# Performance work log

Measured on AMD Instinct MI355X. Metric: run time of the kernel, lower is better.

The kernel has to match this reference:

```python
import jax, jax.numpy as jnp
import numpy as np

D_MODEL = 1024
N_HEADS = 16
HEAD_DIM = D_MODEL // N_HEADS


def setup_inputs() -> dict:
    key = jax.random.key(0)
    ks = jax.random.split(key, 10)
    s = 1.0 / np.sqrt(D_MODEL)
    inp = {
        "ts_features": jax.random.normal(ks[0], (8, 512, D_MODEL), dtype=jnp.float32),
        "llm_features": jax.random.normal(ks[1], (8, 2048, D_MODEL), dtype=jnp.float32),
        "q_w": jax.random.uniform(ks[2], (D_MODEL, D_MODEL), jnp.float32, -s, s),
        "q_b": jax.random.uniform(ks[3], (D_MODEL,), jnp.float32, -s, s),
        "k_w": jax.random.uniform(ks[4], (D_MODEL, D_MODEL), jnp.float32, -s, s),
        "k_b": jax.random.uniform(ks[5], (D_MODEL,), jnp.float32, -s, s),
        "v_w": jax.random.uniform(ks[6], (D_MODEL, D_MODEL), jnp.float32, -s, s),
        "v_b": jax.random.uniform(ks[7], (D_MODEL,), jnp.float32, -s, s),
        "o_w": jax.random.uniform(ks[8], (D_MODEL, D_MODEL), jnp.float32, -s, s),
        "o_b": jax.random.uniform(ks[9], (D_MODEL,), jnp.float32, -s, s),
    }
    return inp


def reference(ts_features, llm_features, q_w, q_b, k_w, k_b, v_w, v_b, o_w, o_b):
    B, P, _ = ts_features.shape
    S = llm_features.shape[1]
    # Linear projections (torch Linear: x @ W^T + b); split heads -> [B, H, L, Dh]
    q = (ts_features @ q_w.T + q_b).reshape(B, P, N_HEADS, HEAD_DIM).transpose(0, 2, 1, 3)
    k = (llm_features @ k_w.T + k_b).reshape(B, S, N_HEADS, HEAD_DIM).transpose(0, 2, 1, 3)
    v = (llm_features @ v_w.T + v_b).reshape(B, S, N_HEADS, HEAD_DIM).transpose(0, 2, 1, 3)
    # Full attention: scores [B, H, P, S]
    scores = jnp.einsum("bhpd,bhsd->bhps", q, k) / np.sqrt(HEAD_DIM).astype(np.float32)
    attn = jax.nn.softmax(scores, axis=-1)  # dropout is identity in eval mode
    context = jnp.einsum("bhps,bhsd->bhpd", attn, v)
    context = context.transpose(0, 2, 1, 3).reshape(B, P, D_MODEL)
    return context @ o_w.T + o_b
```

## Files before the change

### kernel.cpp

```cpp
#include <hip/hip_runtime.h>

#define DM 1024
#define B_ 8
#define P_ 512
#define S_ 2048

typedef __bf16 bf16;
typedef __bf16 bf16x4 __attribute__((ext_vector_type(4)));
typedef __bf16 bf16x8 __attribute__((ext_vector_type(8)));
typedef float f32x4 __attribute__((ext_vector_type(4)));
typedef float f32x16 __attribute__((ext_vector_type(16)));

__device__ __forceinline__ void gload_lds16(const void* g, void* l) {
  __builtin_amdgcn_global_load_lds(
      (const __attribute__((address_space(1))) unsigned int*)g,
      (__attribute__((address_space(3))) unsigned int*)l, 16, 0, 0);
}

__device__ __forceinline__ f32x4 mfma16(bf16x8 a, bf16x8 b, f32x4 c) {
  return __builtin_amdgcn_mfma_f32_16x16x32_bf16(a, b, c, 0, 0, 0);
}
__device__ __forceinline__ f32x16 mfma32(bf16x8 a, bf16x8 b, f32x16 c) {
  return __builtin_amdgcn_mfma_f32_32x32x16_bf16(a, b, c, 0, 0, 0);
}

__device__ __forceinline__ unsigned cvt_pk_bf16(float lo, float hi) {
  unsigned r;
  asm("v_cvt_pk_bf16_f32 %0, %1, %2" : "=v"(r) : "v"(lo), "v"(hi));
  return r;
}
__device__ __forceinline__ void plswap(unsigned& a, unsigned& b) {
  asm volatile("s_nop 1\n\tv_permlane32_swap_b32 %0, %1" : "+v"(a), "+v"(b));
}
__device__ __forceinline__ void bar() {
  asm volatile("" ::: "memory");
  __builtin_amdgcn_s_barrier();
  asm volatile("" ::: "memory");
}

union U8 { unsigned u[4]; bf16x8 v; };

#define QSCALE 0.18033688011112042f

__global__ void cvt_all(const float* __restrict__ ts, const float* __restrict__ llm,
                        const float* __restrict__ qw, const float* __restrict__ kw,
                        const float* __restrict__ vw, const float* __restrict__ ow,
                        bf16* __restrict__ ts_o, bf16* __restrict__ llm_o,
                        bf16* __restrict__ qw_o, bf16* __restrict__ kw_o,
                        bf16* __restrict__ vw_o, bf16* __restrict__ ow_o) {
  const int total = 24 << 18;
  int i = blockIdx.x * blockDim.x + threadIdx.x;
  const int stride = gridDim.x * blockDim.x;
  for (; i < total; i += stride) {
    int r = i >> 18;
    const float* in;
    bf16* out;
    int off;
    if (r < 4) { in = ts; out = ts_o; off = i; }
    else if (r < 20) { in = llm; out = llm_o; off = i - (4 << 18); }
    else if (r == 20) { in = qw; out = qw_o; off = i - (20 << 18); }
    else if (r == 21) { in = kw; out = kw_o; off = i - (21 << 18); }
    else if (r == 22) { in = vw; out = vw_o; off = i - (22 << 18); }
    else { in = ow; out = ow_o; off = i - (23 << 18); }
    float4 v = reinterpret_cast<const float4*>(in)[off];
    bf16x4 o;
    o[0] = (bf16)v.x; o[1] = (bf16)v.y; o[2] = (bf16)v.z; o[3] = (bf16)v.w;
    reinterpret_cast<bf16x4*>(out)[off] = o;
  }
}

enum { MODE_F32 = 0, MODE_Q = 1 };

template <int MODE>
__global__ __launch_bounds__(512) void gemm_bt(
    const bf16* __restrict__ A, const bf16* __restrict__ Bw,
    const float* __restrict__ bias, void* __restrict__ out) {
  __shared__ char As[16384];
  __shared__ char Bs[16384];
  const int tid = threadIdx.x;
  const int w = tid >> 6, lane = tid & 63;
  const int g = lane >> 4, l15 = lane & 15;
  const int tn = blockIdx.x, tm = blockIdx.y;
  const int wm = w >> 2, wn = w & 3;

  f32x4 acc[4][2] = {};

  const char* Abase = (const char*)A + (size_t)(tm * 128) * (DM * 2);
  const char* Bbase = (const char*)Bw + (size_t)(tn * 128) * (DM * 2);

  for (int kt = 0; kt < DM / 64; ++kt) {
#pragma unroll
    for (int i = 0; i < 2; ++i) {
      int f = i * 8192 + (w * 64 + lane) * 16;
      int row = f >> 7;
      int kb = f & 127;
      int src = kb ^ ((row & 7) << 4);
      gload_lds16(Abase + (size_t)row * (DM * 2) + kt * 128 + src,
                  As + i * 8192 + w * 1024);
      gload_lds16(Bbase + (size_t)row * (DM * 2) + kt * 128 + src,
                  Bs + i * 8192 + w * 1024);
    }
    __syncthreads();
#pragma unroll
    for (int kk = 0; kk < 2; ++kk) {
      bf16x8 af[4], bfr[2];
#pragma unroll
      for (int mi = 0; mi < 4; ++mi) {
        int row = wm * 64 + mi * 16 + l15;
        int off = row * 128 + ((kk * 64 + g * 16) ^ ((row & 7) << 4));
        af[mi] = *reinterpret_cast<const bf16x8*>(As + off);
      }
#pragma unroll
      for (int ni = 0; ni < 2; ++ni) {
        int row = wn * 32 + ni * 16 + l15;
        int off = row * 128 + ((kk * 64 + g * 16) ^ ((row & 7) << 4));
        bfr[ni] = *reinterpret_cast<const bf16x8*>(Bs + off);
      }
#pragma unroll
      for (int mi = 0; mi < 4; ++mi)
#pragma unroll
        for (int ni = 0; ni < 2; ++ni)
          acc[mi][ni] = mfma16(af[mi], bfr[ni], acc[mi][ni]);
    }
    __syncthreads();
  }

#pragma unroll
  for (int mi = 0; mi < 4; ++mi) {
#pragma unroll
    for (int ni = 0; ni < 2; ++ni) {
      const int n = tn * 128 + wn * 32 + ni * 16 + l15;
      const float bn = bias[n];
      const int mb = tm * 128 + wm * 64 + mi * 16 + g * 4;
#pragma unroll
      for (int r = 0; r < 4; ++r) {
        const int m = mb + r;
        const float v = acc[mi][ni][r] + bn;
        if constexpr (MODE == MODE_F32) {
          ((float*)out)[(size_t)m * 1024 + n] = v;
        } else {
          const int b = m >> 9, p = m & 511, h = n >> 6, d = n & 63;
          ((bf16*)out)[((size_t)((b * 16 + h) * 512 + p)) * 64 + d] = (bf16)(v * QSCALE);
        }
      }
    }
  }
}

__global__ __launch_bounds__(512, 2) void gemm256kv(
    const bf16* __restrict__ A, const bf16* __restrict__ Bw,
    const float* __restrict__ kb, const float* __restrict__ vb,
    bf16* __restrict__ Kout, bf16* __restrict__ VTout) {
  __shared__ char lds[131072];
  const int tid = threadIdx.x;
  const int w = tid >> 6, lane = tid & 63;
  const int g = lane >> 4, l15 = lane & 15;
  const int wm = w >> 2, wn = w & 3;

  const int id = blockIdx.x;
  const int nid = (id & 7) * 64 + (id >> 3);
  const int tn = nid & 7, tm = nid >> 3;

  const int f0 = tid * 16, f1 = f0 + 8192;
  const int r0 = f0 >> 7, r1 = f1 >> 7;
  const size_t so0 = (size_t)r0 * 2048 + ((f0 & 127) ^ ((r0 & 7) << 4));
  const size_t so1 = (size_t)r1 * 2048 + ((f1 & 127) ^ ((r1 & 7) << 4));

  const char* Ab = (const char*)A + (size_t)(tm * 256) * 2048;
  const char* Bb = (const char*)Bw + (size_t)(tn * 256) * 2048;

#define STG(OP, HALF, KT)                                                      \
  {                                                                            \
    const char* base = ((OP) ? Bb : Ab) + (size_t)((HALF) * 128) * 2048 +      \
                       (size_t)(KT) * 128;                                     \
    char* dst = lds + (OP) * 65536 + ((((KT) & 1) * 2 + (HALF)) * 16384);      \
    gload_lds16(base + so0, dst + f0);                                         \
    gload_lds16(base + so1, dst + f1);                                         \
  }

  f32x4 acc[8][4] = {};
  bf16x8 a[4][2], b0[2][2], b1[2][2];

#define RD_A(MH)                                                               \
  _Pragma("unroll") for (int mi = 0; mi < 4; ++mi) _Pragma("unroll")           \
      for (int kk = 0; kk < 2; ++kk) {                                         \
    int lr = (MH) * 64 + mi * 16 + l15;                                        \
    int off = (((unsigned)(kt & 1) * 2 + wm) * 16384) + lr * 128 +             \
              ((kk * 64 + g * 16) ^ ((lr & 7) << 4));                          \
    a[mi][kk] = *reinterpret_cast<const bf16x8*>(lds + off);                   \
  }
#define RD_B(NH, DST)                                                          \
  _Pragma("unroll") for (int ni = 0; ni < 2; ++ni) _Pragma("unroll")           \
      for (int kk = 0; kk < 2; ++kk) {                                         \
    int lr = (wn & 1) * 64 + ((NH) * 2 + ni) * 16 + l15;                       \
    int off = 65536 + (((unsigned)(kt & 1) * 2 + (wn >> 1)) * 16384) +         \
              lr * 128 + ((kk * 64 + g * 16) ^ ((lr & 7) << 4));               \
    DST[ni][kk] = *reinterpret_cast<const bf16x8*>(lds + off);                 \
  }
#define MM(MH, NH, B)                                                          \
  __builtin_amdgcn_s_setprio(1);                                              \
  _Pragma("unroll") for (int mi = 0; mi < 4; ++mi) _Pragma("unroll")           \
      for (int ni = 0; ni < 2; ++ni) _Pragma("unroll")                         \
      for (int kk = 0; kk < 2; ++kk)                                           \
          acc[(MH)*4 + mi][(NH)*2 + ni] =                                      \
              mfma16(a[mi][kk], B[ni][kk], acc[(MH)*4 + mi][(NH)*2 + ni]);     \
  __builtin_amdgcn_s_setprio(0);

  STG(0, 0, 0); STG(1, 0, 0); STG(0, 1, 0); STG(1, 1, 0);
  STG(1, 1, 1); STG(0, 0, 1); STG(1, 0, 1);
  asm volatile("s_waitcnt vmcnt(6)" ::: "memory");
  bar();

  for (int kt = 0; kt < 16; ++kt) {
    RD_A(0); RD_B(0, b0);
    if (kt + 1 < 16) STG(0, 1, kt + 1);
    bar();
    MM(0, 0, b0);
    bar();
    RD_B(1, b1);
    bar();
    MM(0, 1, b1);
    bar();
    RD_A(1);
    if (kt + 2 < 16) STG(1, 1, kt + 2);
    bar();
    MM(1, 0, b0);
    bar();
    if (kt + 2 < 16) { STG(0, 0, kt + 2); STG(1, 0, kt + 2); }
    if (kt < 14) {
      asm volatile("s_waitcnt vmcnt(6)" ::: "memory");
    } else {
      asm volatile("s_waitcnt vmcnt(0)" ::: "memory");
    }
    bar();
    MM(1, 1, b1);
    bar();
  }

#pragma unroll
  for (int am = 0; am < 8; ++am) {
#pragma unroll
    for (int an = 0; an < 4; ++an) {
      const int n = tn * 256 + wn * 64 + an * 16 + l15;
      const int mb = tm * 256 + wm * 128 + am * 16 + g * 4;
      const int b = mb >> 11, s = mb & 2047;
      if (n >= 1024) {
        const int h = (n - 1024) >> 6, d = (n - 1024) & 63;
        const float bn = vb[n - 1024];
        bf16x4 pk;
#pragma unroll
        for (int r = 0; r < 4; ++r) pk[r] = (bf16)(acc[am][an][r] + bn);
        *reinterpret_cast<bf16x4*>(VTout + ((size_t)((b * 16 + h) * 64 + d)) * 2048 + s) = pk;
      } else {
        const int h = n >> 6, d = n & 63;
        const float bn = kb[n];
#pragma unroll
        for (int r = 0; r < 4; ++r)
          Kout[((size_t)((b * 16 + h) * 2048 + s + r)) * 64 + d] =
              (bf16)(acc[am][an][r] + bn);
      }
    }
  }
#undef STG
#undef RD_A
#undef RD_B
#undef MM
}

__global__ __launch_bounds__(256) void attn_kernel(
    const bf16* __restrict__ Q, const bf16* __restrict__ K,
    const bf16* __restrict__ VT, bf16* __restrict__ ctx) {
  __shared__ char lds[65536];
  const int tid = threadIdx.x;
  const int w = tid >> 6, lane = tid & 63;
  const int l31 = lane & 31, hi = lane >> 5;

  const int n = blockIdx.x;
  const int xcd = n & 7, mm = n >> 3;
  const int bh = xcd + ((mm >> 2) << 3);
  const int qt = mm & 3;
  const int q0 = qt * 128;

  const char* Kb = (const char*)(K + (size_t)bh * 2048 * 64);
  const char* Vb = (const char*)(VT + (size_t)bh * 64 * 2048);

  const char* Qrow = (const char*)(Q + ((size_t)bh * 512 + q0 + w * 32 + l31) * 64);
  bf16x8 qf[4];
#pragma unroll
  for (int kk = 0; kk < 4; ++kk)
    qf[kk] = *reinterpret_cast<const bf16x8*>(Qrow + kk * 32 + hi * 16);

  float lrun = 0.f;
  f32x16 oacc[2] = {};

#define STAGE(S0, BUF)                                                        \
  {                                                                           \
    _Pragma("unroll") for (int i = 0; i < 4; ++i) {                           \
      int f = i * 4096 + (w * 64 + lane) * 16;                                \
      int krow = f >> 7, kbyte = f & 127;                                     \
      gload_lds16(Kb + (size_t)((S0) + krow) * 128 +                          \
                      (kbyte ^ ((krow & 7) << 4)),                            \
                  (BUF) + i * 4096 + w * 1024);                               \
      int vrow = f >> 8, vbyte = f & 255;                                     \
      gload_lds16(Vb + (size_t)vrow * 4096 + (size_t)(S0) * 2 +               \
                      (vbyte ^ ((vrow & 7) << 4)),                            \
                  (BUF) + 16384 + i * 4096 + w * 1024);                       \
    }                                                                         \
  }

#define SUBTILE(T2, CUR)                                                      \
  {                                                                           \
    f32x16 sa[2] = {};                                                        \
    __builtin_amdgcn_s_setprio(1);                                            \
    _Pragma("unroll") for (int t = 0; t < 2; ++t) {                           \
      _Pragma("unroll") for (int kk = 0; kk < 4; ++kk) {                      \
        int row = (T2) * 64 + t * 32 + l31;                                   \
        int off = row * 128 + ((kk * 32 + hi * 16) ^ ((row & 7) << 4));       \
        bf16x8 kf = *reinterpret_cast<const bf16x8*>((CUR) + off);            \
        sa[t] = mfma32(kf, qf[kk], sa[t]);                                    \
      }                                                                       \
    }                                                                         \
    __builtin_amdgcn_s_setprio(0);                                            \
    bf16x8 vf[8];                                                             \
    _Pragma("unroll") for (int dt = 0; dt < 2; ++dt)                          \
        _Pragma("unroll") for (int ks = 0; ks < 4; ++ks) {                    \
      int row = dt * 32 + l31;                                                \
      int col = (T2) * 128 + ks * 32 + hi * 16;                               \
      int off = 16384 + row * 256 + (col ^ ((row & 7) << 4));                 \
      vf[dt * 4 + ks] = *reinterpret_cast<const bf16x8*>((CUR) + off);        \
    }                                                                         \
    bf16x8 pf[4];                                                             \
    _Pragma("unroll") for (int t = 0; t < 2; ++t)                             \
        _Pragma("unroll") for (int h2 = 0; h2 < 2; ++h2) {                    \
      float p[8];                                                             \
      _Pragma("unroll") for (int j = 0; j < 8; ++j) {                         \
        p[j] = __builtin_amdgcn_exp2f(sa[t][8 * h2 + j]);                     \
        lrun += p[j];                                                         \
      }                                                                       \
      unsigned a0 = cvt_pk_bf16(p[0], p[1]);                                  \
      unsigned a1 = cvt_pk_bf16(p[2], p[3]);                                  \
      unsigned a2 = cvt_pk_bf16(p[4], p[5]);                                  \
      unsigned a3 = cvt_pk_bf16(p[6], p[7]);                                  \
      plswap(a0, a2);                                                         \
      plswap(a1, a3);                                                         \
      U8 u;                                                                   \
      u.u[0] = a0; u.u[1] = a1; u.u[2] = a2; u.u[3] = a3;                     \
      pf[t * 2 + h2] = u.v;                                                   \
    }                                                                         \
    __builtin_amdgcn_s_setprio(1);                                            \
    _Pragma("unroll") for (int dt = 0; dt < 2; ++dt)                          \
        _Pragma("unroll") for (int ks = 0; ks < 4; ++ks)                      \
            oacc[dt] = mfma32(vf[dt * 4 + ks], pf[ks], oacc[dt]);             \
    __builtin_amdgcn_s_setprio(0);                                            \
  }

  STAGE(0, lds);

  for (int c = 0; c < 16; ++c) {
    char* cur = lds + (c & 1) * 32768;
    if (c + 1 < 16) {
      STAGE((c + 1) * 128, lds + ((c + 1) & 1) * 32768);
      asm volatile("s_waitcnt vmcnt(8)" ::: "memory");
    } else {
      asm volatile("s_waitcnt vmcnt(0)" ::: "memory");
    }
    bar();

    SUBTILE(0, cur);
    SUBTILE(1, cur);

    bar();
  }

  lrun += __shfl_xor(lrun, 32);
  const float inv = 1.0f / lrun;
  const int b = bh >> 4, h = bh & 15;
  const int prow = q0 + w * 32 + l31;
  bf16* dst = ctx + ((size_t)(b * 512 + prow)) * 1024 + h * 64;
#pragma unroll
  for (int dt = 0; dt < 2; ++dt)
#pragma unroll
    for (int g4 = 0; g4 < 4; ++g4) {
      bf16x4 pk4;
#pragma unroll
      for (int r = 0; r < 4; ++r) pk4[r] = (bf16)(oacc[dt][g4 * 4 + r] * inv);
      *reinterpret_cast<bf16x4*>(dst + dt * 32 + g4 * 8 + hi * 4) = pk4;
    }
#undef STAGE
#undef SUBTILE
}

extern "C" void kernel_launch(void* const* d_in, const int* in_sizes, int n_in,
                              void* d_out, int out_size, void* d_ws, size_t ws_size,
                              hipStream_t stream) {
  const float* ts = (const float*)d_in[0];
  const float* llm = (const float*)d_in[1];
  const float* qw = (const float*)d_in[2];
  const float* qb = (const float*)d_in[3];
  const float* kw = (const float*)d_in[4];
  const float* kb = (const float*)d_in[5];
  const float* vw = (const float*)d_in[6];
  const float* vb = (const float*)d_in[7];
  const float* ow = (const float*)d_in[8];
  const float* ob = (const float*)d_in[9];

  char* ws = (char*)d_ws;
  bf16* ts_bf = (bf16*)(ws + (0ull << 20));
  bf16* llm_bf = (bf16*)(ws + (8ull << 20));
  bf16* qw_bf = (bf16*)(ws + (40ull << 20));
  bf16* kw_bf = (bf16*)(ws + (42ull << 20));
  bf16* vw_bf = (bf16*)(ws + (44ull << 20));
  bf16* ow_bf = (bf16*)(ws + (46ull << 20));
  bf16* Qb = (bf16*)(ws + (48ull << 20));
  bf16* Kb = (bf16*)(ws + (56ull << 20));
  bf16* VTb = (bf16*)(ws + (88ull << 20));
  bf16* ctx = (bf16*)(ws + (120ull << 20));

  cvt_all<<<2048, 256, 0, stream>>>(ts, llm, qw, kw, vw, ow,
                                    ts_bf, llm_bf, qw_bf, kw_bf, vw_bf, ow_bf);

  gemm_bt<MODE_Q><<<dim3(8, 32), 512, 0, stream>>>(ts_bf, qw_bf, qb, Qb);
  gemm256kv<<<512, 512, 0, stream>>>(llm_bf, kw_bf, kb, vb, Kb, VTb);
  attn_kernel<<<512, 256, 0, stream>>>(Qb, Kb, VTb, ctx);
  gemm_bt<MODE_F32><<<dim3(8, 32), 512, 0, stream>>>(ctx, ow_bf, ob, (void*)d_out);
}
```

Before: 188.6 us.

## Replace 256x256 pipelined KV GEMM with simple 128x128 single-buffered tile kernel

Replaces the hand-pipelined 256x256-tile K/V projection GEMM, which double-buffers loads into 128KB of LDS with setprio interleaving, with a plain 128x128-tile kernel. The new kernel uses 32KB of LDS, a single buffer and two syncthreads per k-step, and launches 2048 blocks instead of 512. This gives more blocks and higher occupancy, but halves data reuse per tile and removes the overlap of global loads with MFMA work.

```diff
diff --git a/kernel.cpp b/kernel.cpp
--- a/kernel.cpp
+++ b/kernel.cpp
@@ -147,109 +147,76 @@
   }
 }
 
-__global__ __launch_bounds__(512, 2) void gemm256kv(
+__global__ __launch_bounds__(512) void gemm128kv(
     const bf16* __restrict__ A, const bf16* __restrict__ Bw,
     const float* __restrict__ kb, const float* __restrict__ vb,
     bf16* __restrict__ Kout, bf16* __restrict__ VTout) {
-  __shared__ char lds[131072];
+  __shared__ char As[16384];
+  __shared__ char Bs[16384];
   const int tid = threadIdx.x;
   const int w = tid >> 6, lane = tid & 63;
   const int g = lane >> 4, l15 = lane & 15;
   const int wm = w >> 2, wn = w & 3;
 
   const int id = blockIdx.x;
-  const int nid = (id & 7) * 64 + (id >> 3);
-  const int tn = nid & 7, tm = nid >> 3;
-
-  const int f0 = tid * 16, f1 = f0 + 8192;
-  const int r0 = f0 >> 7, r1 = f1 >> 7;
-  const size_t so0 = (size_t)r0 * 2048 + ((f0 & 127) ^ ((r0 & 7) << 4));
-  const size_t so1 = (size_t)r1 * 2048 + ((f1 & 127) ^ ((r1 & 7) << 4));
-
-  const char* Ab = (const char*)A + (size_t)(tm * 256) * 2048;
-  const char* Bb = (const char*)Bw + (size_t)(tn * 256) * 2048;
-
-#define STG(OP, HALF, KT)                                                      \
-  {                                                                            \
-    const char* base = ((OP) ? Bb : Ab) + (size_t)((HALF) * 128) * 2048 +      \
-                       (size_t)(KT) * 128;                                     \
-    char* dst = lds + (OP) * 65536 + ((((KT) & 1) * 2 + (HALF)) * 16384);      \
-    gload_lds16(base + so0, dst + f0);                                         \
-    gload_lds16(base + so1, dst + f1);                                         \
-  }
-
-  f32x4 acc[8][4] = {};
-  bf16x8 a[4][2], b0[2][2], b1[2][2];
-
-#define RD_A(MH)                                                               \
-  _Pragma("unroll") for (int mi = 0; mi < 4; ++mi) _Pragma("unroll")           \
-      for (int kk = 0; kk < 2; ++kk) {                                         \
-    int lr = (MH) * 64 + mi * 16 + l15;                                        \
-    int off = (((unsigned)(kt & 1) * 2 + wm) * 16384) + lr * 128 +             \
-              ((kk * 64 + g * 16) ^ ((lr & 7) << 4));                          \
-    a[mi][kk] = *reinterpret_cast<const bf16x8*>(lds + off);                   \
-  }
-#define RD_B(NH, DST)                                                          \
-  _Pragma("unroll") for (int ni = 0; ni < 2; ++ni) _Pragma("unroll")           \
-      for (int kk = 0; kk < 2; ++kk) {                                         \
-    int lr = (wn & 1) * 64 + ((NH) * 2 + ni) * 16 + l15;                       \
-    int off = 65536 + (((unsigned)(kt & 1) * 2 + (wn >> 1)) * 16384) +         \
-              lr * 128 + ((kk * 64 + g * 16) ^ ((lr & 7) << 4));               \
-    DST[ni][kk] = *reinterpret_cast<const bf16x8*>(lds + off);                 \
-  }
-#define MM(MH, NH, B)                                                          \
-  __builtin_amdgcn_s_setprio(1);                                              \
-  _Pragma("unroll") for (int mi = 0; mi < 4; ++mi) _Pragma("unroll")           \
-      for (int ni = 0; ni < 2; ++ni) _Pragma("unroll")                         \
-      for (int kk = 0; kk < 2; ++kk)                                           \
-          acc[(MH)*4 + mi][(NH)*2 + ni] =                                      \
-              mfma16(a[mi][kk], B[ni][kk], acc[(MH)*4 + mi][(NH)*2 + ni]);     \
-  __builtin_amdgcn_s_setprio(0);
-
-  STG(0, 0, 0); STG(1, 0, 0); STG(0, 1, 0); STG(1, 1, 0);
-  STG(1, 1, 1); STG(0, 0, 1); STG(1, 0, 1);
-  asm volatile("s_waitcnt vmcnt(6)" ::: "memory");
-  bar();
-
-  for (int kt = 0; kt < 16; ++kt) {
-    RD_A(0); RD_B(0, b0);
-    if (kt + 1 < 16) STG(0, 1, kt + 1);
-    bar();
-    MM(0, 0, b0);
-    bar();
-    RD_B(1, b1);
-    bar();
-    MM(0, 1, b1);
-    bar();
-    RD_A(1);
-    if (kt + 2 < 16) STG(1, 1, kt + 2);
-    bar();
-    MM(1, 0, b0);
-    bar();
-    if (kt + 2 < 16) { STG(0, 0, kt + 2); STG(1, 0, kt + 2); }
-    if (kt < 14) {
-      asm volatile("s_waitcnt vmcnt(6)" ::: "memory");
-    } else {
-      asm volatile("s_waitcnt vmcnt(0)" ::: "memory");
-    }
-    bar();
-    MM(1, 1, b1);
-    bar();
-  }
-
-#pragma unroll
-  for (int am = 0; am < 8; ++am) {
-#pragma unroll
-    for (int an = 0; an < 4; ++an) {
-      const int n = tn * 256 + wn * 64 + an * 16 + l15;
-      const int mb = tm * 256 + wm * 128 + am * 16 + g * 4;
+  const int nid = (id & 7) * 256 + (id >> 3);
+  const int tm = nid >> 4, tn = nid & 15;
+
+  f32x4 acc[4][2] = {};
+
+  const char* Abase = (const char*)A + (size_t)(tm * 128) * (DM * 2);
+  const char* Bbase = (const char*)Bw + (size_t)(tn * 128) * (DM * 2);
+
+  for (int kt = 0; kt < DM / 64; ++kt) {
+#pragma unroll
+    for (int i = 0; i < 2; ++i) {
+      int f = i * 8192 + (w * 64 + lane) * 16;
+      int row = f >> 7;
+      int kb2 = f & 127;
+      int src = kb2 ^ ((row & 7) << 4);
+      gload_lds16(Abase + (size_t)row * (DM * 2) + kt * 128 + src,
+                  As + i * 8192 + w * 1024);
+      gload_lds16(Bbase + (size_t)row * (DM * 2) + kt * 128 + src,
+                  Bs + i * 8192 + w * 1024);
+    }
+    __syncthreads();
+#pragma unroll
+    for (int kk = 0; kk < 2; ++kk) {
+      bf16x8 af[4], bfr[2];
+#pragma unroll
+      for (int mi = 0; mi < 4; ++mi) {
+        int row = wm * 64 + mi * 16 + l15;
+        int off = row * 128 + ((kk * 64 + g * 16) ^ ((row & 7) << 4));
+        af[mi] = *reinterpret_cast<const bf16x8*>(As + off);
+      }
+#pragma unroll
+      for (int ni = 0; ni < 2; ++ni) {
+        int row = wn * 32 + ni * 16 + l15;
+        int off = row * 128 + ((kk * 64 + g * 16) ^ ((row & 7) << 4));
+        bfr[ni] = *reinterpret_cast<const bf16x8*>(Bs + off);
+      }
+#pragma unroll
+      for (int mi = 0; mi < 4; ++mi)
+#pragma unroll
+        for (int ni = 0; ni < 2; ++ni)
+          acc[mi][ni] = mfma16(af[mi], bfr[ni], acc[mi][ni]);
+    }
+    __syncthreads();
+  }
+
+#pragma unroll
+  for (int mi = 0; mi < 4; ++mi) {
+#pragma unroll
+    for (int ni = 0; ni < 2; ++ni) {
+      const int n = tn * 128 + wn * 32 + ni * 16 + l15;
+      const int mb = tm * 128 + wm * 64 + mi * 16 + g * 4;
       const int b = mb >> 11, s = mb & 2047;
       if (n >= 1024) {
         const int h = (n - 1024) >> 6, d = (n - 1024) & 63;
         const float bn = vb[n - 1024];
         bf16x4 pk;
 #pragma unroll
-        for (int r = 0; r < 4; ++r) pk[r] = (bf16)(acc[am][an][r] + bn);
+        for (int r = 0; r < 4; ++r) pk[r] = (bf16)(acc[mi][ni][r] + bn);
         *reinterpret_cast<bf16x4*>(VTout + ((size_t)((b * 16 + h) * 64 + d)) * 2048 + s) = pk;
       } else {
         const int h = n >> 6, d = n & 63;
@@ -257,14 +224,10 @@
 #pragma unroll
         for (int r = 0; r < 4; ++r)
           Kout[((size_t)((b * 16 + h) * 2048 + s + r)) * 64 + d] =
-              (bf16)(acc[am][an][r] + bn);
-      }
-    }
-  }
-#undef STG
-#undef RD_A
-#undef RD_B
-#undef MM
+              (bf16)(acc[mi][ni][r] + bn);
+      }
+    }
+  }
 }
 
 __global__ __launch_bounds__(256) void attn_kernel(
@@ -420,7 +383,7 @@
                                     ts_bf, llm_bf, qw_bf, kw_bf, vw_bf, ow_bf);
 
   gemm_bt<MODE_Q><<<dim3(8, 32), 512, 0, stream>>>(ts_bf, qw_bf, qb, Qb);
-  gemm256kv<<<512, 512, 0, stream>>>(llm_bf, kw_bf, kb, vb, Kb, VTb);
+  gemm128kv<<<2048, 512, 0, stream>>>(llm_bf, kw_bf, kb, vb, Kb, VTb);
   attn_kernel<<<512, 256, 0, stream>>>(Qb, Kb, VTb, ctx);
   gemm_bt<MODE_F32><<<dim3(8, 32), 512, 0, stream>>>(ctx, ow_bf, ob, (void*)d_out);
 }
```

New measurement: 189.2 us. Within noise of the previous version (+0.3%).
